# Kernel tuning notes

Measured on AMD Instinct MI355X. Metric: run time of the kernel, lower is better.

The kernel has to match this reference:

```python
import jax, jax.numpy as jnp
import numpy as np
import math

HIDDEN = 1024
NUM_HEADS = 16
NUM_GROUPS = 16  # source einsum/rearrange only shape-checks when groups == heads
HEAD_DIM = HIDDEN // NUM_HEADS


def rope(x, base=10000.0):
    # x: [b, s, d]; applied to the FULL hidden vector before head split, as in source.
    # Source rope_fn has a reshape bug; this is the intended rotate-half RoPE with
    # half_d frequencies 1/base^(i/half_d) (== 1/base^(2i/d)).
    b, s, d = x.shape
    half = d // 2
    x1, x2 = x[..., :half], x[..., half:]
    pos = jnp.arange(s, dtype=x.dtype)[:, None]                          # [s,1]
    inv_freq = 1.0 / (base ** (jnp.arange(half, dtype=x.dtype) / half))  # [half]
    ang = pos * inv_freq[None, :]                                        # [s,half]
    sin = jnp.sin(ang)[None]                                             # [1,s,half]
    cos = jnp.cos(ang)[None]
    return jnp.concatenate([x1 * cos - x2 * sin, x2 * cos + x1 * sin], axis=-1)


def setup_inputs() -> dict:
    key = jax.random.key(0)
    ks = jax.random.split(key, 10)
    scale = 1.0 / math.sqrt(HIDDEN)
    inp = {
        "x": jax.random.normal(ks[0], (2, 2048, HIDDEN), dtype=jnp.float32),
        "attn_mask": jax.random.randint(ks[1], (2, 2048), 0, 2, dtype=jnp.int32),
        "Wq": jax.random.uniform(ks[2], (HIDDEN, HIDDEN), jnp.float32, -scale, scale),
        "bq": jax.random.uniform(ks[3], (HIDDEN,), jnp.float32, -scale, scale),
        "Wk": jax.random.uniform(ks[4], (HIDDEN, HIDDEN), jnp.float32, -scale, scale),
        "bk": jax.random.uniform(ks[5], (HIDDEN,), jnp.float32, -scale, scale),
        "Wv": jax.random.uniform(ks[6], (HIDDEN, HIDDEN), jnp.float32, -scale, scale),
        "bv": jax.random.uniform(ks[7], (HIDDEN,), jnp.float32, -scale, scale),
        "Wo": jax.random.uniform(ks[8], (HIDDEN, HIDDEN), jnp.float32, -scale, scale),
        "bo": jax.random.uniform(ks[9], (HIDDEN,), jnp.float32, -scale, scale),
    }
    return inp


def reference(x, attn_mask, Wq, bq, Wk, bk, Wv, bv, Wo, bo):
    b, s, _ = x.shape
    g = NUM_GROUPS
    subh = NUM_HEADS // g  # = 1 here
    d = HIDDEN // g        # per-group dim (== head dim when g == h)

    q = rope(x @ Wq.T + bq)
    k = rope(x @ Wk.T + bk)
    v = x @ Wv.T + bv

    # q: b s (g subh d) -> b g subh s d ; k,v: b s (g d) -> b g s d
    q = q.reshape(b, s, g, subh, d).transpose(0, 2, 3, 1, 4)
    k = k.reshape(b, s, g, d).transpose(0, 2, 1, 3)
    v = v.reshape(b, s, g, d).transpose(0, 2, 1, 3)

    e = jnp.einsum('bghqd,bgkd->bghqk', q, k) / math.sqrt(HEAD_DIM)  # [b,g,subh,s,s]
    mask5 = attn_mask[:, None, None, None, :]  # broadcast over g, subh, query
    e = jnp.where(mask5 == 0, -jnp.inf, e)
    attn = jax.nn.softmax(e, axis=-1)
    out = jnp.einsum('bghqk,bgkd->bghqd', attn, v)            # [b,g,subh,s,d]
    out = out.transpose(0, 3, 1, 2, 4).reshape(b, s, HIDDEN)  # b s (g subh d)
    return out @ Wo.T + bo
```

## Files before the change

### kernel.cpp

```cpp
#include <hip/hip_runtime.h>
#include <hip/hip_bf16.h>


constexpr int Bb  = 2;
constexpr int Ss  = 2048;
constexpr int Hh  = 1024;
constexpr int NHh = 16;
constexpr int Mm  = Bb * Ss;

typedef __attribute__((ext_vector_type(8))) unsigned short ushort8;
typedef __attribute__((ext_vector_type(8))) short short8;
typedef __attribute__((ext_vector_type(4))) float f32x4;
typedef __attribute__((ext_vector_type(4))) unsigned int u32x4;

__device__ __forceinline__ unsigned short f2bf(float f) {
    unsigned int u = __float_as_uint(f);
    u += 0x7fffu + ((u >> 16) & 1u);
    return (unsigned short)(u >> 16);
}
__device__ __forceinline__ float bf2f(unsigned short h) {
    return __uint_as_float(((unsigned int)h) << 16);
}
__device__ __forceinline__ void gload16(const void* g, void* l) {
    __builtin_amdgcn_global_load_lds(
        (const __attribute__((address_space(1))) unsigned int*)g,
        (__attribute__((address_space(3))) unsigned int*)l, 16, 0, 0);
}

__global__ __launch_bounds__(256) void convert_k(
    const float* __restrict__ x,
    const float* __restrict__ Wq, const float* __restrict__ Wk,
    const float* __restrict__ Wv, const float* __restrict__ Wo,
    unsigned short* __restrict__ xb, unsigned short* __restrict__ wall)
{
    size_t e = ((size_t)blockIdx.x * 256 + threadIdx.x) << 3;
    const float* s; unsigned short* d;
    if (e < (size_t)Mm * Hh) {
        s = x + e; d = xb + e;
    } else {
        size_t f = e - (size_t)Mm * Hh;
        int t = (int)(f >> 20);
        const float* w = (t == 0) ? Wq : (t == 1) ? Wk : (t == 2) ? Wv : Wo;
        s = w + (f & 1048575);
        d = wall + f;
    }
    float4 a = *(const float4*)s;
    float4 b = *(const float4*)(s + 4);
    ushort8 o;
    o[0] = f2bf(a.x); o[1] = f2bf(a.y); o[2] = f2bf(a.z); o[3] = f2bf(a.w);
    o[4] = f2bf(b.x); o[5] = f2bf(b.y); o[6] = f2bf(b.z); o[7] = f2bf(b.w);
    *(ushort8*)d = o;
}

__global__ __launch_bounds__(256) void maskbf_k(
    const int* __restrict__ am, unsigned short* __restrict__ maskbf)
{
    int i = blockIdx.x * 256 + threadIdx.x;
    maskbf[i] = am[i] ? (unsigned short)0x3F80 : (unsigned short)0;
}

#define GEMM_BODY(ATYPE_PTR, WPTR, K0MAX)                                          \
    __shared__ unsigned short As[128 * 64];                                        \
    __shared__ unsigned short Bs[128 * 64];                                        \
    const int tid  = threadIdx.x;                                                  \
    const int lane = tid & 63;                                                     \
    const int w    = tid >> 6;                                                     \
    const int wr   = w >> 1, wc = w & 1;                                           \
    const int l16  = lane & 15, g = lane >> 4;                                     \
    const int R0   = blockIdx.x * 128;                                             \
    char* asb = (char*)As; char* bsb = (char*)Bs;                                  \
    f32x4 acc[4][4] = {};                                                          \
    for (int k0 = 0; k0 < K0MAX; k0 += 64) {                                       \
        _Pragma("unroll")                                                          \
        for (int it = 0; it < 4; ++it) {                                           \
            int sbase = w * 4096 + it * 1024;                                      \
            int boff  = sbase + lane * 16;                                         \
            int r     = boff >> 7;                                                 \
            int c     = (boff >> 4) & 7;                                           \
            int col   = k0 + ((c ^ (r & 7)) << 3);                                 \
            gload16(&ATYPE_PTR[(size_t)(R0 + r) * 1024 + col], asb + sbase);       \
            gload16(&WPTR[(size_t)(gn + r) * 1024 + col], bsb + sbase);            \
        }                                                                          \
        __syncthreads();                                                           \
        short8 bfrag[4][2];                                                        \
        _Pragma("unroll")                                                          \
        for (int u = 0; u < 4; ++u) {                                              \
            int row = wc * 64 + u * 16 + l16;                                      \
            _Pragma("unroll")                                                      \
            for (int s = 0; s < 2; ++s)                                            \
                bfrag[u][s] = *(const short8*)(bsb + row * 128 +                   \
                               ((s * 64 + g * 16) ^ ((row & 7) << 4)));            \
        }                                                                          \
        _Pragma("unroll")                                                          \
        for (int t = 0; t < 4; ++t) {                                              \
            int row = wr * 64 + t * 16 + l16;                                      \
            short8 af[2];                                                          \
            _Pragma("unroll")                                                      \
            for (int s = 0; s < 2; ++s)                                            \
                af[s] = *(const short8*)(asb + row * 128 +                         \
                         ((s * 64 + g * 16) ^ ((row & 7) << 4)));                  \
            _Pragma("unroll")                                                      \
            for (int u = 0; u < 4; ++u) {                                          \
                acc[t][u] = __builtin_amdgcn_mfma_f32_16x16x32_bf16(af[0], bfrag[u][0], acc[t][u], 0, 0, 0); \
                acc[t][u] = __builtin_amdgcn_mfma_f32_16x16x32_bf16(af[1], bfrag[u][1], acc[t][u], 0, 0, 0); \
            }                                                                      \
        }                                                                          \
        __syncthreads();                                                           \
    }

__global__ __launch_bounds__(256) void gemm_qkv_k(
    const unsigned short* __restrict__ xb, const unsigned short* __restrict__ wall,
    const float* __restrict__ bq, const float* __restrict__ bk, const float* __restrict__ bv,
    unsigned short* __restrict__ q, unsigned short* __restrict__ k2,
    unsigned short* __restrict__ v)
{
    const int gn = blockIdx.y * 128;
    GEMM_BODY(xb, wall, 1024)

    const int sel = gn >> 10;
    const int n0  = gn & 1023;
    const float* bias = (sel == 0) ? bq : (sel == 1) ? bk : bv;
    unsigned short* outp = (sel == 0) ? q : (sel == 1) ? k2 : v;
    const float qs = (sel == 0) ? 0.18033688011112042f : 1.0f;
    #pragma unroll
    for (int u = 0; u < 4; ++u) {
        int coll = wc * 64 + u * 16 + l16;
        float bb = bias[n0 + coll];
        #pragma unroll
        for (int t = 0; t < 4; ++t)
            #pragma unroll
            for (int rr = 0; rr < 4; ++rr) {
                int row = R0 + wr * 64 + t * 16 + g * 4 + rr;
                outp[(size_t)row * 1024 + n0 + coll] = f2bf((acc[t][u][rr] + bb) * qs);
            }
    }
}

__global__ __launch_bounds__(256) void gemm_out_k(
    const unsigned short* __restrict__ ao, const unsigned short* __restrict__ wo,
    const float* __restrict__ bo, float* __restrict__ out)
{
    const int gn = blockIdx.y * 128;
    GEMM_BODY(ao, wo, 1024)

    #pragma unroll
    for (int u = 0; u < 4; ++u) {
        int coll = wc * 64 + u * 16 + l16;
        float bb = bo[gn + coll];
        #pragma unroll
        for (int t = 0; t < 4; ++t)
            #pragma unroll
            for (int rr = 0; rr < 4; ++rr) {
                int row = R0 + wr * 64 + t * 16 + g * 4 + rr;
                out[(size_t)row * 1024 + gn + coll] = acc[t][u][rr] + bb;
            }
    }
}

__global__ __launch_bounds__(256) void rope_frag_k(
    const unsigned short* __restrict__ qin, const unsigned short* __restrict__ kin,
    unsigned short* __restrict__ qfrag, unsigned short* __restrict__ kfrag)
{
    __shared__ unsigned short Ld[2][64][72];
    const int kt = blockIdx.x;
    const int hp = blockIdx.y;
    const int zz = blockIdx.z;
    const int bz = zz & 1, sel = zz >> 1;
    const unsigned short* src = sel ? kin : qin;
    unsigned short* dstf = sel ? kfrag : qfrag;

    const int t   = threadIdx.x;
    const int r   = t & 63;
    const int c16 = (t >> 6) << 4;
    const int pos = kt * 64 + r;
    const size_t rowb = (size_t)(bz * Ss + pos) * 1024;

    ushort8 A0 = *(const ushort8*)&src[rowb + hp * 64 + c16];
    ushort8 A1 = *(const ushort8*)&src[rowb + hp * 64 + c16 + 8];
    ushort8 B0 = *(const ushort8*)&src[rowb + (hp + 8) * 64 + c16];
    ushort8 B1 = *(const ushort8*)&src[rowb + (hp + 8) * 64 + c16 + 8];

    #pragma unroll
    for (int i = 0; i < 16; ++i) {
        int d = c16 + i;
        float jj  = (float)(hp * 64 + d);
        float inv = exp2f(jj * -0.0259525632621414f);
        float ang = (float)pos * inv;
        float sn, cs;
        __sincosf(ang, &sn, &cs);
        unsigned short ua = (i < 8) ? A0[i] : A1[i - 8];
        unsigned short ub = (i < 8) ? B0[i] : B1[i - 8];
        float a = bf2f(ua), b = bf2f(ub);
        Ld[0][r][d] = f2bf(a * cs - b * sn);
        Ld[1][r][d] = f2bf(b * cs + a * sn);
    }
    __syncthreads();

    #pragma unroll
    for (int cc = 0; cc < 4; ++cc) {
        int c    = t * 4 + cc;
        int hh   = c >> 9;
        int ci   = c & 511;
        int blk  = ci >> 7, s2 = (ci >> 6) & 1, lane2 = ci & 63;
        int gg = lane2 >> 4, ll = lane2 & 15;
        ushort8 o = *(const ushort8*)&Ld[hh][blk * 16 + ll][s2 * 32 + gg * 8];
        size_t base = (size_t)(bz * 16 + hp + hh * 8) * 131072 + (size_t)kt * 4096;
        *(ushort8*)&dstf[base + (size_t)ci * 8] = o;
    }
}

__global__ __launch_bounds__(256) void fragify_v_k(
    const unsigned short* __restrict__ v, const int* __restrict__ mask,
    unsigned short* __restrict__ vfrag)
{
    __shared__ unsigned short Ld[64][72];
    __shared__ int Lm[64];
    const int kt = blockIdx.x, bh = blockIdx.y;
    const int bz = bh >> 4, h = bh & 15;
    const int t = threadIdx.x;
    const int r = t & 63, c0 = (t >> 6) << 4;
    const unsigned short* srcp = &v[(size_t)(bz * Ss + kt * 64 + r) * 1024 + h * 64 + c0];
    *(ushort8*)&Ld[r][c0]     = *(const ushort8*)srcp;
    *(ushort8*)&Ld[r][c0 + 8] = *(const ushort8*)(srcp + 8);
    if (t < 64) Lm[t] = mask[bz * Ss + kt * 64 + t];
    __syncthreads();

    #pragma unroll
    for (int cc = 0; cc < 2; ++cc) {
        int c = t * 2 + cc;
        int dt4 = c >> 7, ks = (c >> 6) & 1, lane2 = c & 63;
        int gg = lane2 >> 4, ll = lane2 & 15;
        ushort8 o;
        #pragma unroll
        for (int e = 0; e < 8; ++e) {
            int key = ks * 32 + gg * 8 + e;
            o[e] = Lm[key] ? Ld[key][dt4 * 16 + ll] : (unsigned short)0;
        }
        *(ushort8*)&vfrag[(size_t)bh * 131072 + (size_t)kt * 4096 + (size_t)c * 8] = o;
    }
}

__global__ __launch_bounds__(256, 4) void flash_k(
    const unsigned short* __restrict__ qfrag, const unsigned short* __restrict__ kfrag,
    const unsigned short* __restrict__ vfrag, const unsigned short* __restrict__ maskbf,
    unsigned short* __restrict__ opart, float2* __restrict__ ml)
{
    const int F    = blockIdx.x;
    const int xcd  = F & 7, j = F >> 3;
    const int grp  = xcd * 4 + (j >> 6);
    const int rem  = j & 63;
    const int qb   = rem >> 1;
    const int half = rem & 1;
    const int h    = grp & 15;
    const int bz   = grp >> 4;
    const int kt0  = half * 16;

    const int tid  = threadIdx.x;
    const int lane = tid & 63;
    const int w    = tid >> 6;
    const int l16  = lane & 15;
    const int g    = lane >> 4;

    const size_t fb = (size_t)(bz * 16 + h) * 131072;
    const unsigned short* kfb = kfrag + fb;
    const unsigned short* vfb = vfrag + fb;
    const unsigned short* qfb = qfrag + fb;
    const unsigned short* mbz = maskbf + bz * Ss;

    short8 qf0 = *(const short8*)&qfb[(size_t)(qb * 4 + w) * 1024 + lane * 8];
    short8 qf1 = *(const short8*)&qfb[(size_t)(qb * 4 + w) * 1024 + 512 + lane * 8];

    f32x4 O[4];
    #pragma unroll
    for (int d = 0; d < 4; ++d) O[d] = (f32x4)0.f;
    f32x4 Osum = (f32x4)0.f;
    float mrow = -1.0e4f;

    for (int kt = kt0; kt < kt0 + 16; ++kt) {
        short8 KC[8];
        #pragma unroll
        for (int i = 0; i < 8; ++i)
            KC[i] = *(const short8*)&kfb[(size_t)kt * 4096 + i * 512 + lane * 8];
        short8 mf0 = *(const short8*)&mbz[kt * 64 + g * 8];
        short8 mf1 = *(const short8*)&mbz[kt * 64 + 32 + g * 8];

        f32x4 S[4];
        #pragma unroll
        for (int k4 = 0; k4 < 4; ++k4) S[k4] = (f32x4)0.f;
        #pragma unroll
        for (int k4 = 0; k4 < 4; ++k4) {
            S[k4] = __builtin_amdgcn_mfma_f32_16x16x32_bf16(KC[k4 * 2 + 0], qf0, S[k4], 0, 0, 0);
            S[k4] = __builtin_amdgcn_mfma_f32_16x16x32_bf16(KC[k4 * 2 + 1], qf1, S[k4], 0, 0, 0);
        }

        short8 V0[4];
        #pragma unroll
        for (int dt = 0; dt < 4; ++dt)
            V0[dt] = *(const short8*)&vfb[(size_t)kt * 4096 + (dt * 2) * 512 + lane * 8];

        float m0 = fmaxf(fmaxf(S[0][0], S[0][1]), fmaxf(S[0][2], S[0][3]));
        float m1 = fmaxf(fmaxf(S[1][0], S[1][1]), fmaxf(S[1][2], S[1][3]));
        float m2 = fmaxf(fmaxf(S[2][0], S[2][1]), fmaxf(S[2][2], S[2][3]));
        float m3 = fmaxf(fmaxf(S[3][0], S[3][1]), fmaxf(S[3][2], S[3][3]));
        float m  = fmaxf(fmaxf(m0, m1), fmaxf(m2, m3));
        m = fmaxf(m, __shfl_xor(m, 16));
        m = fmaxf(m, __shfl_xor(m, 32));

        if (__any((int)(m > mrow + 10.0f))) {
            float mn = fmaxf(mrow, m);
            float rs = exp2f(mrow - mn);
            mrow = mn;
            #pragma unroll
            for (int r = 0; r < 4; ++r) {
                float f0 = __shfl(rs, g * 4 + r);
                #pragma unroll
                for (int dt = 0; dt < 4; ++dt) O[dt][r] *= f0;
                Osum[r] *= f0;
            }
        }

        unsigned int U[4][2];
        #pragma unroll
        for (int k4 = 0; k4 < 4; ++k4) {
            float p0 = exp2f(S[k4][0] - mrow);
            float p1 = exp2f(S[k4][1] - mrow);
            float p2 = exp2f(S[k4][2] - mrow);
            float p3 = exp2f(S[k4][3] - mrow);
            asm("v_cvt_pk_bf16_f32 %0, %1, %2" : "=v"(U[k4][0]) : "v"(p0), "v"(p1));
            asm("v_cvt_pk_bf16_f32 %0, %1, %2" : "=v"(U[k4][1]) : "v"(p2), "v"(p3));
        }
        asm("v_permlane32_swap_b32 %0, %1" : "+v"(U[0][0]), "+v"(U[1][0]));
        asm("v_permlane32_swap_b32 %0, %1" : "+v"(U[0][1]), "+v"(U[1][1]));
        asm("v_permlane32_swap_b32 %0, %1" : "+v"(U[2][0]), "+v"(U[3][0]));
        asm("v_permlane32_swap_b32 %0, %1" : "+v"(U[2][1]), "+v"(U[3][1]));
        asm("v_permlane16_swap_b32 %0, %1" : "+v"(U[0][0]), "+v"(U[1][0]));
        asm("v_permlane16_swap_b32 %0, %1" : "+v"(U[0][1]), "+v"(U[1][1]));
        asm("v_permlane16_swap_b32 %0, %1" : "+v"(U[2][0]), "+v"(U[3][0]));
        asm("v_permlane16_swap_b32 %0, %1" : "+v"(U[2][1]), "+v"(U[3][1]));

        u32x4 gp0, gp1;
        gp0[0] = U[0][0]; gp0[1] = U[0][1]; gp0[2] = U[1][0]; gp0[3] = U[1][1];
        gp1[0] = U[2][0]; gp1[1] = U[2][1]; gp1[2] = U[3][0]; gp1[3] = U[3][1];
        short8 pf0 = __builtin_bit_cast(short8, gp0);
        short8 pf1 = __builtin_bit_cast(short8, gp1);

        Osum = __builtin_amdgcn_mfma_f32_16x16x32_bf16(pf0, mf0, Osum, 0, 0, 0);
        #pragma unroll
        for (int dt = 0; dt < 4; ++dt)
            O[dt] = __builtin_amdgcn_mfma_f32_16x16x32_bf16(pf0, V0[dt], O[dt], 0, 0, 0);

        short8 V1[4];
        #pragma unroll
        for (int dt = 0; dt < 4; ++dt)
            V1[dt] = *(const short8*)&vfb[(size_t)kt * 4096 + (dt * 2 + 1) * 512 + lane * 8];
        Osum = __builtin_amdgcn_mfma_f32_16x16x32_bf16(pf1, mf1, Osum, 0, 0, 0);
        #pragma unroll
        for (int dt = 0; dt < 4; ++dt)
            O[dt] = __builtin_amdgcn_mfma_f32_16x16x32_bf16(pf1, V1[dt], O[dt], 0, 0, 0);
    }

    const size_t NE = (size_t)Mm * Hh;
    #pragma unroll
    for (int r = 0; r < 4; ++r) {
        float osum = Osum[r];
        float inv  = osum > 0.f ? 1.0f / osum : 0.f;
        float mo   = __shfl(mrow, g * 4 + r);
        int rowl   = qb * 64 + w * 16 + g * 4 + r;
        size_t ob  = (size_t)half * NE + ((size_t)(bz * Ss + rowl)) * 1024 + h * 64;
        #pragma unroll
        for (int dt = 0; dt < 4; ++dt)
            opart[ob + dt * 16 + l16] = f2bf(O[dt][r] * inv);
        if (l16 == 0)
            ml[((half * 2 + bz) * 16 + h) * 2048 + rowl] = make_float2(mo, osum);
    }
}

__global__ __launch_bounds__(256) void combine_k(
    const unsigned short* __restrict__ opart, const float2* __restrict__ ml,
    unsigned short* __restrict__ ao)
{
    const size_t NE = (size_t)Mm * Hh;
    int c    = blockIdx.x * 256 + threadIdx.x;
    int row  = c >> 7;
    int col8 = c & 127;
    int h    = col8 >> 3;
    int bz   = row >> 11, qrow = row & 2047;

    float2 a = ml[((0 * 2 + bz) * 16 + h) * 2048 + qrow];
    float2 b = ml[((1 * 2 + bz) * 16 + h) * 2048 + qrow];
    float M  = fmaxf(a.x, b.x);
    float w1 = exp2f(a.x - M) * a.y;
    float w2 = exp2f(b.x - M) * b.y;
    float tot = w1 + w2;
    float inv = tot > 0.f ? 1.0f / tot : 0.f;
    w1 *= inv; w2 *= inv;

    ushort8 o1 = *(const ushort8*)&opart[(size_t)c * 8];
    ushort8 o2 = *(const ushort8*)&opart[NE + (size_t)c * 8];
    ushort8 o;
    #pragma unroll
    for (int jj = 0; jj < 8; ++jj)
        o[jj] = f2bf(bf2f(o1[jj]) * w1 + bf2f(o2[jj]) * w2);
    *(ushort8*)&ao[(size_t)c * 8] = o;
}

extern "C" void kernel_launch(void* const* d_in, const int* in_sizes, int n_in,
                              void* d_out, int out_size, void* d_ws, size_t ws_size,
                              hipStream_t stream)
{
    const float* x  = (const float*)d_in[0];
    const int*   am = (const int*)d_in[1];
    const float* Wq = (const float*)d_in[2];
    const float* bq = (const float*)d_in[3];
    const float* Wk = (const float*)d_in[4];
    const float* bk = (const float*)d_in[5];
    const float* Wv = (const float*)d_in[6];
    const float* bv = (const float*)d_in[7];
    const float* Wo = (const float*)d_in[8];
    const float* bo = (const float*)d_in[9];
    float* out = (float*)d_out;

    const size_t NE = (size_t)Mm * Hh;
    unsigned short* q     = (unsigned short*)d_ws;
    unsigned short* k     = q + NE;
    unsigned short* v     = k + NE;
    unsigned short* ao    = v + NE;
    unsigned short* xb    = ao + NE;
    unsigned short* wall  = xb + NE;
    unsigned short* wo    = wall + 3u * 1048576u;
    unsigned short* kfrag = wall + 4u * 1048576u;
    unsigned short* qfrag = xb;
    unsigned short* vfrag = q;
    unsigned short* opart = k;
    float2*         ml    = (float2*)(kfrag + 4u * 1048576u);
    unsigned short* maskbf = (unsigned short*)(ml + 131072);

    convert_k<<<(2 * NE) / (256 * 8), 256, 0, stream>>>(x, Wq, Wk, Wv, Wo, xb, wall);
    maskbf_k<<<dim3(Mm / 256), 256, 0, stream>>>(am, maskbf);
    gemm_qkv_k<<<dim3(Mm / 128, 3072 / 128), 256, 0, stream>>>(
        xb, wall, bq, bk, bv, q, k, v);
    rope_frag_k<<<dim3(32, 8, 4), 256, 0, stream>>>(q, k, qfrag, kfrag);
    fragify_v_k<<<dim3(32, 32), 256, 0, stream>>>(v, am, vfrag);
    flash_k<<<dim3(2048), 256, 0, stream>>>(qfrag, kfrag, vfrag, maskbf, opart, ml);
    combine_k<<<dim3((Mm * 128) / 256), 256, 0, stream>>>(opart, ml, ao);
    gemm_out_k<<<dim3(Mm / 128, Hh / 128), 256, 0, stream>>>(ao, wo, bo, out);
}
```

Measured before the change: 175.0 us.

## Process two query tiles per wave in flash kernel to reuse K/V fragments

Each wave now handles two 16-row query tiles instead of one, so every K, V and mask fragment loaded from global memory feeds twice as many MFMAs. The grid is halved to 1024 blocks, block-to-work mapping is adjusted, and launch bounds drop to 3 waves per SIMD to make room for the doubled accumulator and score registers. The intent is to cut K/V load traffic per unit of compute. The cost is lower occupancy and fewer blocks, which may reduce latency hiding.

```diff
diff --git a/kernel.cpp b/kernel.cpp
--- a/kernel.cpp
+++ b/kernel.cpp
@@ -240,20 +240,20 @@
     }
 }
 
-__global__ __launch_bounds__(256, 4) void flash_k(
+__global__ __launch_bounds__(256, 3) void flash_k(
     const unsigned short* __restrict__ qfrag, const unsigned short* __restrict__ kfrag,
     const unsigned short* __restrict__ vfrag, const unsigned short* __restrict__ maskbf,
     unsigned short* __restrict__ opart, float2* __restrict__ ml)
 {
-    const int F    = blockIdx.x;
-    const int xcd  = F & 7, j = F >> 3;
-    const int grp  = xcd * 4 + (j >> 6);
-    const int rem  = j & 63;
-    const int qb   = rem >> 1;
+    const int F   = blockIdx.x;
+    const int xcd = F & 7, j = F >> 3;
+    const int grp = xcd * 4 + (j >> 5);
+    const int rem = j & 31;
+    const int qb  = rem >> 1;
     const int half = rem & 1;
-    const int h    = grp & 15;
-    const int bz   = grp >> 4;
-    const int kt0  = half * 16;
+    const int h   = grp & 15;
+    const int bz  = grp >> 4;
+    const int kt0 = half * 16;
 
     const int tid  = threadIdx.x;
     const int lane = tid & 63;
@@ -265,114 +265,147 @@
     const unsigned short* kfb = kfrag + fb;
     const unsigned short* vfb = vfrag + fb;
     const unsigned short* qfb = qfrag + fb;
-    const unsigned short* mbz = maskbf + bz * Ss;
-
-    short8 qf0 = *(const short8*)&qfb[(size_t)(qb * 4 + w) * 1024 + lane * 8];
-    short8 qf1 = *(const short8*)&qfb[(size_t)(qb * 4 + w) * 1024 + 512 + lane * 8];
-
-    f32x4 O[4];
-    #pragma unroll
-    for (int d = 0; d < 4; ++d) O[d] = (f32x4)0.f;
-    f32x4 Osum = (f32x4)0.f;
-    float mrow = -1.0e4f;
-
-    for (int kt = kt0; kt < kt0 + 16; ++kt) {
+
+    const unsigned short* kp = kfb + (size_t)kt0 * 4096 + lane * 8;
+    const unsigned short* vp = vfb + (size_t)kt0 * 4096 + lane * 8;
+    const unsigned short* mp = maskbf + bz * Ss + kt0 * 64 + g * 8;
+
+    short8 qf[2][2];
+    #pragma unroll
+    for (int t = 0; t < 2; ++t)
+        #pragma unroll
+        for (int s = 0; s < 2; ++s)
+            qf[t][s] = *(const short8*)&qfb[(size_t)(qb * 8 + w * 2 + t) * 1024
+                                            + s * 512 + lane * 8];
+
+    f32x4 O[2][4];
+    #pragma unroll
+    for (int t = 0; t < 2; ++t)
+        #pragma unroll
+        for (int d = 0; d < 4; ++d) O[t][d] = (f32x4)0.f;
+    f32x4 Osum[2];
+    Osum[0] = (f32x4)0.f; Osum[1] = (f32x4)0.f;
+    float mrow[2] = {-1.0e4f, -1.0e4f};
+    const f32x4 Zf = (f32x4)0.f;
+
+    for (int it = 0; it < 16; ++it) {
         short8 KC[8];
         #pragma unroll
-        for (int i = 0; i < 8; ++i)
-            KC[i] = *(const short8*)&kfb[(size_t)kt * 4096 + i * 512 + lane * 8];
-        short8 mf0 = *(const short8*)&mbz[kt * 64 + g * 8];
-        short8 mf1 = *(const short8*)&mbz[kt * 64 + 32 + g * 8];
-
-        f32x4 S[4];
-        #pragma unroll
-        for (int k4 = 0; k4 < 4; ++k4) S[k4] = (f32x4)0.f;
-        #pragma unroll
-        for (int k4 = 0; k4 < 4; ++k4) {
-            S[k4] = __builtin_amdgcn_mfma_f32_16x16x32_bf16(KC[k4 * 2 + 0], qf0, S[k4], 0, 0, 0);
-            S[k4] = __builtin_amdgcn_mfma_f32_16x16x32_bf16(KC[k4 * 2 + 1], qf1, S[k4], 0, 0, 0);
+        for (int i = 0; i < 4; ++i) KC[i]     = *(const short8*)(kp + i * 512);
+        #pragma unroll
+        for (int i = 0; i < 4; ++i) KC[4 + i] = *(const short8*)(kp + 2048 + i * 512);
+        short8 mf[2];
+        mf[0] = *(const short8*)mp;
+        mf[1] = *(const short8*)(mp + 32);
+
+        f32x4 S[2][4];
+        #pragma unroll
+        for (int k4 = 0; k4 < 4; ++k4)
+            #pragma unroll
+            for (int t = 0; t < 2; ++t) {
+                S[t][k4] = __builtin_amdgcn_mfma_f32_16x16x32_bf16(
+                    KC[k4 * 2 + 0], qf[t][0], Zf, 0, 0, 0);
+                S[t][k4] = __builtin_amdgcn_mfma_f32_16x16x32_bf16(
+                    KC[k4 * 2 + 1], qf[t][1], S[t][k4], 0, 0, 0);
+            }
+
+        short8 V0[4];
+        #pragma unroll
+        for (int dt = 0; dt < 4; ++dt)
+            V0[dt] = *(const short8*)(vp + dt * 1024);
+
+        float rm[2];
+        #pragma unroll
+        for (int t = 0; t < 2; ++t) {
+            float m0 = fmaxf(fmaxf(S[t][0][0], S[t][0][1]), fmaxf(S[t][0][2], S[t][0][3]));
+            float m1 = fmaxf(fmaxf(S[t][1][0], S[t][1][1]), fmaxf(S[t][1][2], S[t][1][3]));
+            float m2 = fmaxf(fmaxf(S[t][2][0], S[t][2][1]), fmaxf(S[t][2][2], S[t][2][3]));
+            float m3 = fmaxf(fmaxf(S[t][3][0], S[t][3][1]), fmaxf(S[t][3][2], S[t][3][3]));
+            float m  = fmaxf(fmaxf(m0, m1), fmaxf(m2, m3));
+            m = fmaxf(m, __shfl_xor(m, 16));
+            m = fmaxf(m, __shfl_xor(m, 32));
+            rm[t] = m;
         }
 
-        short8 V0[4];
-        #pragma unroll
-        for (int dt = 0; dt < 4; ++dt)
-            V0[dt] = *(const short8*)&vfb[(size_t)kt * 4096 + (dt * 2) * 512 + lane * 8];
-
-        float m0 = fmaxf(fmaxf(S[0][0], S[0][1]), fmaxf(S[0][2], S[0][3]));
-        float m1 = fmaxf(fmaxf(S[1][0], S[1][1]), fmaxf(S[1][2], S[1][3]));
-        float m2 = fmaxf(fmaxf(S[2][0], S[2][1]), fmaxf(S[2][2], S[2][3]));
-        float m3 = fmaxf(fmaxf(S[3][0], S[3][1]), fmaxf(S[3][2], S[3][3]));
-        float m  = fmaxf(fmaxf(m0, m1), fmaxf(m2, m3));
-        m = fmaxf(m, __shfl_xor(m, 16));
-        m = fmaxf(m, __shfl_xor(m, 32));
-
-        if (__any((int)(m > mrow + 10.0f))) {
-            float mn = fmaxf(mrow, m);
-            float rs = exp2f(mrow - mn);
-            mrow = mn;
+        bool grow = (rm[0] > mrow[0] + 10.0f) || (rm[1] > mrow[1] + 10.0f);
+        if (__any((int)grow)) {
+            float mn0 = fmaxf(mrow[0], rm[0]);
+            float mn1 = fmaxf(mrow[1], rm[1]);
+            float rs0 = exp2f(mrow[0] - mn0);
+            float rs1 = exp2f(mrow[1] - mn1);
+            mrow[0] = mn0; mrow[1] = mn1;
             #pragma unroll
             for (int r = 0; r < 4; ++r) {
-                float f0 = __shfl(rs, g * 4 + r);
+                float f0 = __shfl(rs0, g * 4 + r);
+                float f1 = __shfl(rs1, g * 4 + r);
                 #pragma unroll
-                for (int dt = 0; dt < 4; ++dt) O[dt][r] *= f0;
-                Osum[r] *= f0;
+                for (int dt = 0; dt < 4; ++dt) { O[0][dt][r] *= f0; O[1][dt][r] *= f1; }
+                Osum[0][r] *= f0; Osum[1][r] *= f1;
             }
         }
 
-        unsigned int U[4][2];
-        #pragma unroll
-        for (int k4 = 0; k4 < 4; ++k4) {
-            float p0 = exp2f(S[k4][0] - mrow);
-            float p1 = exp2f(S[k4][1] - mrow);
-            float p2 = exp2f(S[k4][2] - mrow);
-            float p3 = exp2f(S[k4][3] - mrow);
-            asm("v_cvt_pk_bf16_f32 %0, %1, %2" : "=v"(U[k4][0]) : "v"(p0), "v"(p1));
-            asm("v_cvt_pk_bf16_f32 %0, %1, %2" : "=v"(U[k4][1]) : "v"(p2), "v"(p3));
+        short8 V1[4];
+        #pragma unroll
+        for (int dt = 0; dt < 4; ++dt)
+            V1[dt] = *(const short8*)(vp + 512 + dt * 1024);
+
+        #pragma unroll
+        for (int t = 0; t < 2; ++t) {
+            unsigned int U[4][2];
+            #pragma unroll
+            for (int k4 = 0; k4 < 4; ++k4) {
+                float p0 = exp2f(S[t][k4][0] - mrow[t]);
+                float p1 = exp2f(S[t][k4][1] - mrow[t]);
+                float p2 = exp2f(S[t][k4][2] - mrow[t]);
+                float p3 = exp2f(S[t][k4][3] - mrow[t]);
+                asm("v_cvt_pk_bf16_f32 %0, %1, %2" : "=v"(U[k4][0]) : "v"(p0), "v"(p1));
+                asm("v_cvt_pk_bf16_f32 %0, %1, %2" : "=v"(U[k4][1]) : "v"(p2), "v"(p3));
+            }
+            asm("v_permlane32_swap_b32 %0, %1" : "+v"(U[0][0]), "+v"(U[1][0]));
+            asm("v_permlane32_swap_b32 %0, %1" : "+v"(U[0][1]), "+v"(U[1][1]));
+            asm("v_permlane32_swap_b32 %0, %1" : "+v"(U[2][0]), "+v"(U[3][0]));
+            asm("v_permlane32_swap_b32 %0, %1" : "+v"(U[2][1]), "+v"(U[3][1]));
+            asm("v_permlane16_swap_b32 %0, %1" : "+v"(U[0][0]), "+v"(U[1][0]));
+            asm("v_permlane16_swap_b32 %0, %1" : "+v"(U[0][1]), "+v"(U[1][1]));
+            asm("v_permlane16_swap_b32 %0, %1" : "+v"(U[2][0]), "+v"(U[3][0]));
+            asm("v_permlane16_swap_b32 %0, %1" : "+v"(U[2][1]), "+v"(U[3][1]));
+
+            u32x4 gp0, gp1;
+            gp0[0] = U[0][0]; gp0[1] = U[0][1]; gp0[2] = U[1][0]; gp0[3] = U[1][1];
+            gp1[0] = U[2][0]; gp1[1] = U[2][1]; gp1[2] = U[3][0]; gp1[3] = U[3][1];
+            short8 pf0 = __builtin_bit_cast(short8, gp0);
+            short8 pf1 = __builtin_bit_cast(short8, gp1);
+
+            Osum[t] = __builtin_amdgcn_mfma_f32_16x16x32_bf16(pf0, mf[0], Osum[t], 0, 0, 0);
+            #pragma unroll
+            for (int dt = 0; dt < 4; ++dt)
+                O[t][dt] = __builtin_amdgcn_mfma_f32_16x16x32_bf16(pf0, V0[dt], O[t][dt], 0, 0, 0);
+            Osum[t] = __builtin_amdgcn_mfma_f32_16x16x32_bf16(pf1, mf[1], Osum[t], 0, 0, 0);
+            #pragma unroll
+            for (int dt = 0; dt < 4; ++dt)
+                O[t][dt] = __builtin_amdgcn_mfma_f32_16x16x32_bf16(pf1, V1[dt], O[t][dt], 0, 0, 0);
         }
-        asm("v_permlane32_swap_b32 %0, %1" : "+v"(U[0][0]), "+v"(U[1][0]));
-        asm("v_permlane32_swap_b32 %0, %1" : "+v"(U[0][1]), "+v"(U[1][1]));
-        asm("v_permlane32_swap_b32 %0, %1" : "+v"(U[2][0]), "+v"(U[3][0]));
-        asm("v_permlane32_swap_b32 %0, %1" : "+v"(U[2][1]), "+v"(U[3][1]));
-        asm("v_permlane16_swap_b32 %0, %1" : "+v"(U[0][0]), "+v"(U[1][0]));
-        asm("v_permlane16_swap_b32 %0, %1" : "+v"(U[0][1]), "+v"(U[1][1]));
-        asm("v_permlane16_swap_b32 %0, %1" : "+v"(U[2][0]), "+v"(U[3][0]));
-        asm("v_permlane16_swap_b32 %0, %1" : "+v"(U[2][1]), "+v"(U[3][1]));
-
-        u32x4 gp0, gp1;
-        gp0[0] = U[0][0]; gp0[1] = U[0][1]; gp0[2] = U[1][0]; gp0[3] = U[1][1];
-        gp1[0] = U[2][0]; gp1[1] = U[2][1]; gp1[2] = U[3][0]; gp1[3] = U[3][1];
-        short8 pf0 = __builtin_bit_cast(short8, gp0);
-        short8 pf1 = __builtin_bit_cast(short8, gp1);
-
-        Osum = __builtin_amdgcn_mfma_f32_16x16x32_bf16(pf0, mf0, Osum, 0, 0, 0);
-        #pragma unroll
-        for (int dt = 0; dt < 4; ++dt)
-            O[dt] = __builtin_amdgcn_mfma_f32_16x16x32_bf16(pf0, V0[dt], O[dt], 0, 0, 0);
-
-        short8 V1[4];
-        #pragma unroll
-        for (int dt = 0; dt < 4; ++dt)
-            V1[dt] = *(const short8*)&vfb[(size_t)kt * 4096 + (dt * 2 + 1) * 512 + lane * 8];
-        Osum = __builtin_amdgcn_mfma_f32_16x16x32_bf16(pf1, mf1, Osum, 0, 0, 0);
-        #pragma unroll
-        for (int dt = 0; dt < 4; ++dt)
-            O[dt] = __builtin_amdgcn_mfma_f32_16x16x32_bf16(pf1, V1[dt], O[dt], 0, 0, 0);
+
+        kp += 4096; vp += 4096; mp += 64;
     }
 
     const size_t NE = (size_t)Mm * Hh;
     #pragma unroll
-    for (int r = 0; r < 4; ++r) {
-        float osum = Osum[r];
-        float inv  = osum > 0.f ? 1.0f / osum : 0.f;
-        float mo   = __shfl(mrow, g * 4 + r);
-        int rowl   = qb * 64 + w * 16 + g * 4 + r;
-        size_t ob  = (size_t)half * NE + ((size_t)(bz * Ss + rowl)) * 1024 + h * 64;
-        #pragma unroll
-        for (int dt = 0; dt < 4; ++dt)
-            opart[ob + dt * 16 + l16] = f2bf(O[dt][r] * inv);
-        if (l16 == 0)
-            ml[((half * 2 + bz) * 16 + h) * 2048 + rowl] = make_float2(mo, osum);
-    }
+    for (int t = 0; t < 2; ++t)
+        #pragma unroll
+        for (int r = 0; r < 4; ++r) {
+            float osum = Osum[t][r];
+            float inv  = osum > 0.f ? 1.0f / osum : 0.f;
+            float mo   = __shfl(mrow[t], g * 4 + r);
+            int rowl   = qb * 128 + w * 32 + t * 16 + g * 4 + r;
+            size_t ob  = (size_t)half * NE
+                       + ((size_t)(bz * Ss + rowl)) * 1024 + h * 64;
+            #pragma unroll
+            for (int dt = 0; dt < 4; ++dt)
+                opart[ob + dt * 16 + l16] = f2bf(O[t][dt][r] * inv);
+            if (l16 == 0)
+                ml[((half * 2 + bz) * 16 + h) * 2048 + rowl] = make_float2(mo, osum);
+        }
 }
 
 __global__ __launch_bounds__(256) void combine_k(
@@ -441,7 +474,7 @@
         xb, wall, bq, bk, bv, q, k, v);
     rope_frag_k<<<dim3(32, 8, 4), 256, 0, stream>>>(q, k, qfrag, kfrag);
     fragify_v_k<<<dim3(32, 32), 256, 0, stream>>>(v, am, vfrag);
-    flash_k<<<dim3(2048), 256, 0, stream>>>(qfrag, kfrag, vfrag, maskbf, opart, ml);
+    flash_k<<<dim3(1024), 256, 0, stream>>>(qfrag, kfrag, vfrag, maskbf, opart, ml);
     combine_k<<<dim3((Mm * 128) / 256), 256, 0, stream>>>(opart, ml, ao);
     gemm_out_k<<<dim3(Mm / 128, Hh / 128), 256, 0, stream>>>(ao, wo, bo, out);
 }
```

Result: faster. 164.9 us (-5.8%).
